# Kernel optimization log

Hardware: AMD Instinct MI355X
Metric: run time of the kernel (lower is better)

The kernel has to match this reference:

```python
import jax, jax.numpy as jnp
import numpy as np
from jax import lax


def setup_inputs() -> dict:
    key = jax.random.key(0)
    k1, k2 = jax.random.split(key)
    B, C_out, C_in, K, H, W = 16, 128, 128, 3, 64, 64
    features = jax.random.normal(k1, (B, C_in, H, W), dtype=jnp.float32)
    dynamic_kernel = jax.random.normal(k2, (B, C_out, C_in, K, K), dtype=jnp.float32)
    return {"features": features, "dynamic_kernel": dynamic_kernel}


def reference(features, dynamic_kernel):
    # Per-sample dynamic conv. unfold+bmm in torch == cross-correlation (conv2d)
    # with the per-sample kernel; we express it as a vmapped implicit-GEMM conv
    # instead of materializing the (C_in*K*K, H*W) unfold buffer.
    padding = 1

    def conv_one(x, w):  # x: (C_in, H, W), w: (C_out, C_in, K, K)
        return lax.conv_general_dilated(
            x[None],                      # (1, C_in, H, W)
            w,
            window_strides=(1, 1),
            padding=[(padding, padding), (padding, padding)],
            dimension_numbers=("NCHW", "OIHW", "NCHW"),
        )[0]                              # (C_out, H, W)

    return jax.vmap(conv_one)(features, dynamic_kernel)  # (B, C_out, H, W)
```

## Files before the change

kernel.cpp:

```cpp
#include <hip/hip_runtime.h>
#include <stdint.h>

#define BATCH 16
#define CIN   128
#define COUT  128
#define IMG_H 64
#define IMG_W 64
#define HW    4096
#define KTOT  1152
#define XH    66
#define XW    66
#define NCQ   16
#define BM    128
#define BN    64
#define BK    64
#define NSTEPS 18
#define ASTEP 8192
#define BSTEP 4096

typedef __attribute__((ext_vector_type(8))) __bf16 bf16x8;
typedef __attribute__((ext_vector_type(4))) float  f32x4;
typedef __attribute__((address_space(1))) const void* gas_p;
typedef __attribute__((address_space(3))) void*       las_p;

static __device__ __forceinline__ unsigned short f2bf(float f) {
  union { float f; uint32_t u; } c; c.f = f;
  uint32_t r = c.u + 0x7fffu + ((c.u >> 16) & 1u);
  return (unsigned short)(r >> 16);
}

static __device__ __forceinline__ void gload_lds16(const unsigned short* g, unsigned short* l) {
  __builtin_amdgcn_global_load_lds((gas_p)g, (las_p)l, 16, 0, 0);
}

__global__ void prep_fused(const float* __restrict__ x, const float* __restrict__ w,
                           unsigned short* __restrict__ wt4, unsigned short* __restrict__ xpad) {
  const int t = threadIdx.x;
  if (blockIdx.x < BATCH * IMG_H) {
    __shared__ uint32_t tile[64 * 68];
    const int b = blockIdx.x & 15;
    const int h = blockIdx.x >> 4;
    const float* xb = x + (size_t)b * CIN * HW + h * IMG_W;
    uint4* xp4 = (uint4*)xpad;

    const int lane16 = t & 15;
    const int g      = t >> 4;
#pragma unroll
    for (int it = 0; it < 4; ++it) {
      const int ci = it * 32 + g * 2;
      const float4 va = *(const float4*)(xb + (size_t)ci * HW + lane16 * 4);
      const float4 vb = *(const float4*)(xb + (size_t)(ci + 1) * HW + lane16 * 4);
      const float av[4] = {va.x, va.y, va.z, va.w};
      const float bv[4] = {vb.x, vb.y, vb.z, vb.w};
#pragma unroll
      for (int cc = 0; cc < 4; ++cc)
        tile[(lane16 * 4 + cc) * 68 + it * 16 + g] =
            (uint32_t)f2bf(av[cc]) | ((uint32_t)f2bf(bv[cc]) << 16);
    }
    __syncthreads();

    const uint32_t rbase = ((uint32_t)b * XH + h + 1) * NCQ;
#pragma unroll
    for (int it = 0; it < 4; ++it) {
      const int o   = it * 256 + t;
      const int cqg = o >> 6;
      const int wc  = o & 63;
      const uint4 v = *(const uint4*)&tile[wc * 68 + cqg * 4];
      xp4[(rbase + cqg) * XW + wc + 1] = v;
    }
    if (t < 32) {
      const int cqg = t & 15;
      const int col = (t >> 4) ? 65 : 0;
      xp4[(rbase + cqg) * XW + col] = make_uint4(0, 0, 0, 0);
    }
    if (h == 0) {
      const uint32_t r0  = (uint32_t)b * XH * NCQ * XW;
      const uint32_t r65 = ((uint32_t)b * XH + 65) * NCQ * XW;
      for (int i = t; i < NCQ * XW; i += 256) {
        xp4[r0 + i]  = make_uint4(0, 0, 0, 0);
        xp4[r65 + i] = make_uint4(0, 0, 0, 0);
      }
    }
  } else {
    const int idx  = blockIdx.x - BATCH * IMG_H;
    const int b    = idx & 15;
    const int step = idx >> 4;
    const int khkw = step >> 1;
    const int cib  = (step & 1) << 6;
    const float* wb = w + (size_t)b * COUT * KTOT;
    unsigned short* dst = wt4 + ((size_t)b * NSTEPS + step) * ASTEP;
#pragma unroll
    for (int i = 0; i < 4; ++i) {
      const int c  = i * 256 + t;
      const int cq = c >> 7;
      const int co = c & 127;
      const int ci0 = cib + cq * 8;
      const float* src = wb + (size_t)co * KTOT + (size_t)ci0 * 9 + khkw;
      uint32_t p[4];
#pragma unroll
      for (int e = 0; e < 4; ++e)
        p[e] = (uint32_t)f2bf(src[(2 * e) * 9]) | ((uint32_t)f2bf(src[(2 * e + 1) * 9]) << 16);
      *(uint4*)&dst[(size_t)c * 8] = make_uint4(p[0], p[1], p[2], p[3]);
    }
  }
}

__global__ __launch_bounds__(256, 4) void dynconv_gemm(
    const unsigned short* __restrict__ wt4,
    const unsigned short* __restrict__ xpad,
    float* __restrict__ out) {
  __shared__ alignas(16) unsigned short As[ASTEP];
  __shared__ alignas(16) unsigned short Bs[BSTEP];

  const int t    = threadIdx.x;
  const int b    = blockIdx.x & 15;
  const int oh   = blockIdx.x >> 4;

  const int lane = t & 63;
  const int wave = t >> 6;
  const int wm   = (wave & 1) << 6;
  const int wn   = (wave >> 1) << 5;
  const int l15  = lane & 15;
  const int quad = lane >> 4;

  const unsigned short* abase = wt4 + (size_t)b * NSTEPS * ASTEP + (size_t)t * 8;
  const unsigned short* xb = xpad + (size_t)b * XH * NCQ * XW * 8;
  const unsigned short* bbase[2];
#pragma unroll
  for (int i = 0; i < 2; ++i)
    bbase[i] = xb + (size_t)(((i * 4 + wave) * XW) + lane) * 8;

  unsigned short* alds[4];
  unsigned short* blds[2];
#pragma unroll
  for (int i = 0; i < 4; ++i) alds[i] = &As[(i * 256 + wave * 64) * 8];
#pragma unroll
  for (int i = 0; i < 2; ++i) blds[i] = &Bs[((i * 4 + wave) * 64) * 8];

  f32x4 acc[4][2] = {};

  for (int step = 0; step < NSTEPS; ++step) {
    const int khkw = step >> 1;
    const int kh   = (khkw * 11) >> 5;
    const int kw   = khkw - kh * 3;
    const size_t boff = ((size_t)((oh + kh) * NCQ + ((step & 1) << 3)) * XW + kw) * 8;
    const unsigned short* astep = abase + (size_t)step * ASTEP;

#pragma unroll
    for (int i = 0; i < 4; ++i) gload_lds16(astep + i * 2048, alds[i]);
#pragma unroll
    for (int i = 0; i < 2; ++i) gload_lds16(bbase[i] + boff, blds[i]);
    __syncthreads();

#pragma unroll
    for (int ks = 0; ks < 2; ++ks) {
      const int cq = ks * 4 + quad;
      bf16x8 af[4], bf[2];
#pragma unroll
      for (int i = 0; i < 4; ++i) af[i] = *(const bf16x8*)&As[(cq * 128 + wm + i * 16 + l15) * 8];
#pragma unroll
      for (int j = 0; j < 2; ++j) bf[j] = *(const bf16x8*)&Bs[(cq * 64 + wn + j * 16 + l15) * 8];
#pragma unroll
      for (int i = 0; i < 4; ++i)
#pragma unroll
        for (int j = 0; j < 2; ++j)
          acc[i][j] = __builtin_amdgcn_mfma_f32_16x16x32_bf16(af[i], bf[j], acc[i][j], 0, 0, 0);
    }
    __syncthreads();
  }

  float* obase = out + (size_t)b * COUT * HW + oh * 64;
#pragma unroll
  for (int i = 0; i < 4; ++i) {
#pragma unroll
    for (int r = 0; r < 4; ++r) {
      const int row = wm + i * 16 + quad * 4 + r;
      float* orow = obase + (size_t)row * HW;
#pragma unroll
      for (int j = 0; j < 2; ++j)
        orow[wn + j * 16 + l15] = acc[i][j][r];
    }
  }
}

__global__ void dynconv_naive(const float* __restrict__ x, const float* __restrict__ w,
                              float* __restrict__ out) {
  const int o   = blockIdx.x * 256 + threadIdx.x;
  const int pix = o & (HW - 1);
  const int co  = (o >> 12) & (COUT - 1);
  const int b   = o >> 19;
  const int oh  = pix >> 6, ow = pix & 63;
  const float* xb = x + (size_t)b * CIN * HW;
  const float* wb = w + ((size_t)b * COUT + co) * CIN * 9;
  float s = 0.f;
  for (int ci = 0; ci < CIN; ++ci) {
    const float* xc = xb + ci * HW;
    const float* wc = wb + ci * 9;
#pragma unroll
    for (int kh = 0; kh < 3; ++kh) {
      const int ih = oh + kh - 1;
      if ((unsigned)ih >= IMG_H) continue;
#pragma unroll
      for (int kw = 0; kw < 3; ++kw) {
        const int iw = ow + kw - 1;
        if ((unsigned)iw >= IMG_W) continue;
        s += xc[ih * IMG_W + iw] * wc[kh * 3 + kw];
      }
    }
  }
  out[o] = s;
}

extern "C" void kernel_launch(void* const* d_in, const int* in_sizes, int n_in,
                              void* d_out, int out_size, void* d_ws, size_t ws_size,
                              hipStream_t stream) {
  const float* x = (const float*)d_in[0];
  const float* w = (const float*)d_in[1];
  float* out = (float*)d_out;

  const size_t wt_bytes = (size_t)BATCH * NSTEPS * ASTEP * sizeof(unsigned short);
  const size_t xp_bytes = (size_t)BATCH * XH * NCQ * XW * 8 * sizeof(unsigned short);

  if (ws_size >= wt_bytes + xp_bytes) {
    unsigned short* wt4  = (unsigned short*)d_ws;
    unsigned short* xpad = (unsigned short*)((char*)d_ws + wt_bytes);
    prep_fused<<<BATCH * IMG_H + BATCH * NSTEPS, 256, 0, stream>>>(x, w, wt4, xpad);
    dynconv_gemm<<<IMG_H * BATCH, 256, 0, stream>>>(wt4, xpad, out);
  } else {
    dynconv_naive<<<(BATCH * COUT * HW) / 256, 256, 0, stream>>>(x, w, out);
  }
}
```

Measured before the change: 123.7 us.

## Stage input slab once in LDS, stream weights into registers with double buffering

Each GEMM block now covers two output rows. It loads the four padded input rows it needs (all channels) into LDS once and takes the kw shifts from that slab with clamped and zeroed edge columns, so it no longer reloads the B tile every step. Weight fragments are read directly from global memory into registers with a two-deep software pipeline, which removes the per-step LDS staging and the two barriers per step. The cost is higher register pressure (16 accumulators, 16 A fragments), occupancy dropping to 2 blocks per CU, and half as many blocks.

```diff
diff --git a/kernel.cpp b/kernel.cpp
--- a/kernel.cpp
+++ b/kernel.cpp
@@ -11,12 +11,8 @@
 #define XH    66
 #define XW    66
 #define NCQ   16
-#define BM    128
-#define BN    64
-#define BK    64
 #define NSTEPS 18
 #define ASTEP 8192
-#define BSTEP 4096
 
 typedef __attribute__((ext_vector_type(8))) __bf16 bf16x8;
 typedef __attribute__((ext_vector_type(4))) float  f32x4;
@@ -27,6 +23,11 @@
   union { float f; uint32_t u; } c; c.f = f;
   uint32_t r = c.u + 0x7fffu + ((c.u >> 16) & 1u);
   return (unsigned short)(r >> 16);
+}
+
+static __device__ __forceinline__ bf16x8 ldg8(const unsigned short* p) {
+  uint4 w = *(const uint4*)p;
+  return __builtin_bit_cast(bf16x8, w);
 }
 
 static __device__ __forceinline__ void gload_lds16(const unsigned short* g, unsigned short* l) {
@@ -105,80 +106,90 @@
   }
 }
 
-__global__ __launch_bounds__(256, 4) void dynconv_gemm(
+__global__ __launch_bounds__(256, 2) void dynconv_gemm(
     const unsigned short* __restrict__ wt4,
     const unsigned short* __restrict__ xpad,
     float* __restrict__ out) {
-  __shared__ alignas(16) unsigned short As[ASTEP];
-  __shared__ alignas(16) unsigned short Bs[BSTEP];
+  __shared__ alignas(16) unsigned short slab[4 * NCQ * 64 * 8];
 
   const int t    = threadIdx.x;
-  const int b    = blockIdx.x & 15;
-  const int oh   = blockIdx.x >> 4;
+  const int b    = blockIdx.y;
+  const int oh0  = blockIdx.x * 2;
 
   const int lane = t & 63;
   const int wave = t >> 6;
   const int wm   = (wave & 1) << 6;
-  const int wn   = (wave >> 1) << 5;
+  const int osub = wave >> 1;
   const int l15  = lane & 15;
   const int quad = lane >> 4;
 
-  const unsigned short* abase = wt4 + (size_t)b * NSTEPS * ASTEP + (size_t)t * 8;
-  const unsigned short* xb = xpad + (size_t)b * XH * NCQ * XW * 8;
-  const unsigned short* bbase[2];
-#pragma unroll
-  for (int i = 0; i < 2; ++i)
-    bbase[i] = xb + (size_t)(((i * 4 + wave) * XW) + lane) * 8;
-
-  unsigned short* alds[4];
-  unsigned short* blds[2];
-#pragma unroll
-  for (int i = 0; i < 4; ++i) alds[i] = &As[(i * 256 + wave * 64) * 8];
-#pragma unroll
-  for (int i = 0; i < 2; ++i) blds[i] = &Bs[((i * 4 + wave) * 64) * 8];
-
-  f32x4 acc[4][2] = {};
-
-  for (int step = 0; step < NSTEPS; ++step) {
-    const int khkw = step >> 1;
-    const int kh   = (khkw * 11) >> 5;
-    const int kw   = khkw - kh * 3;
-    const size_t boff = ((size_t)((oh + kh) * NCQ + ((step & 1) << 3)) * XW + kw) * 8;
-    const unsigned short* astep = abase + (size_t)step * ASTEP;
-
-#pragma unroll
-    for (int i = 0; i < 4; ++i) gload_lds16(astep + i * 2048, alds[i]);
-#pragma unroll
-    for (int i = 0; i < 2; ++i) gload_lds16(bbase[i] + boff, blds[i]);
-    __syncthreads();
-
-#pragma unroll
-    for (int ks = 0; ks < 2; ++ks) {
-      const int cq = ks * 4 + quad;
-      bf16x8 af[4], bf[2];
-#pragma unroll
-      for (int i = 0; i < 4; ++i) af[i] = *(const bf16x8*)&As[(cq * 128 + wm + i * 16 + l15) * 8];
-#pragma unroll
-      for (int j = 0; j < 2; ++j) bf[j] = *(const bf16x8*)&Bs[(cq * 64 + wn + j * 16 + l15) * 8];
-#pragma unroll
-      for (int i = 0; i < 4; ++i)
-#pragma unroll
-        for (int j = 0; j < 2; ++j)
-          acc[i][j] = __builtin_amdgcn_mfma_f32_16x16x32_bf16(af[i], bf[j], acc[i][j], 0, 0, 0);
-    }
-    __syncthreads();
-  }
-
-  float* obase = out + (size_t)b * COUT * HW + oh * 64;
+  {
+    const unsigned short* xsrc = xpad +
+        ((((size_t)b * XH + oh0) * NCQ) * XW + 1 + lane) * 8;
+#pragma unroll
+    for (int p = 0; p < 16; ++p) {
+      const int seg = p * 4 + wave;
+      gload_lds16(xsrc + (size_t)seg * XW * 8, &slab[(p * 256 + wave * 64) * 8]);
+    }
+  }
+  __syncthreads();
+
+  const unsigned short* wbase = wt4 + (size_t)b * NSTEPS * ASTEP + (size_t)(quad * 128 + wm + l15) * 8;
+
+  f32x4 acc[4][4] = {};
+  bf16x8 afA[8], afB[8];
+
+#define LOADA(S, AF)                                                          \
+  {                                                                           \
+    const unsigned short* wstep_ = wbase + (size_t)(S) * ASTEP;               \
+    _Pragma("unroll") for (int ks_ = 0; ks_ < 2; ++ks_)                       \
+      _Pragma("unroll") for (int i_ = 0; i_ < 4; ++i_)                        \
+        AF[ks_ * 4 + i_] = ldg8(wstep_ + (ks_ * 512 + i_ * 16) * 8);          \
+  }
+
+#define COMPUTE(S, AF)                                                        \
+  {                                                                           \
+    const int khkw_ = (S) >> 1;                                               \
+    const int kh_ = khkw_ / 3, kw_ = khkw_ % 3;                               \
+    _Pragma("unroll") for (int ks_ = 0; ks_ < 2; ++ks_) {                     \
+      const int cq_ = ((S) & 1) * 8 + ks_ * 4 + quad;                         \
+      const int rb_ = ((osub + kh_) * NCQ + cq_) * 64;                        \
+      bf16x8 bf[4];                                                           \
+      _Pragma("unroll") for (int j_ = 0; j_ < 4; ++j_) {                      \
+        int cm_ = j_ * 16 + l15 + kw_ - 1;                                    \
+        if (j_ == 0) cm_ = cm_ < 0 ? 0 : cm_;                                 \
+        if (j_ == 3) cm_ = cm_ > 63 ? 63 : cm_;                               \
+        bf[j_] = *(const bf16x8*)&slab[(rb_ + cm_) * 8];                      \
+      }                                                                       \
+      if (kw_ == 0 && l15 == 0)  bf[0] = (bf16x8){};                          \
+      if (kw_ == 2 && l15 == 15) bf[3] = (bf16x8){};                          \
+      _Pragma("unroll") for (int i_ = 0; i_ < 4; ++i_)                        \
+        _Pragma("unroll") for (int j_ = 0; j_ < 4; ++j_)                      \
+          acc[i_][j_] = __builtin_amdgcn_mfma_f32_16x16x32_bf16(              \
+              AF[ks_ * 4 + i_], bf[j_], acc[i_][j_], 0, 0, 0);                \
+    }                                                                         \
+  }
+
+  LOADA(0, afA);
+#pragma unroll
+  for (int s = 0; s < NSTEPS; s += 2) {
+    LOADA(s + 1, afB);
+    COMPUTE(s, afA);
+    if (s + 2 < NSTEPS) LOADA(s + 2, afA);
+    COMPUTE(s + 1, afB);
+  }
+#undef LOADA
+#undef COMPUTE
+
+  float* obase = out + (size_t)b * COUT * HW + (oh0 + osub) * 64;
 #pragma unroll
   for (int i = 0; i < 4; ++i) {
 #pragma unroll
     for (int r = 0; r < 4; ++r) {
-      const int row = wm + i * 16 + quad * 4 + r;
-      float* orow = obase + (size_t)row * HW;
-#pragma unroll
-      for (int j = 0; j < 2; ++j)
-        orow[wn + j * 16 + l15] = acc[i][j][r];
+      float* orow = obase + (size_t)(wm + i * 16 + quad * 4 + r) * HW;
+#pragma unroll
+      for (int j = 0; j < 4; ++j)
+        orow[j * 16 + l15] = acc[i][j][r];
     }
   }
 }
@@ -225,7 +236,8 @@
     unsigned short* wt4  = (unsigned short*)d_ws;
     unsigned short* xpad = (unsigned short*)((char*)d_ws + wt_bytes);
     prep_fused<<<BATCH * IMG_H + BATCH * NSTEPS, 256, 0, stream>>>(x, w, wt4, xpad);
-    dynconv_gemm<<<IMG_H * BATCH, 256, 0, stream>>>(wt4, xpad, out);
+    dim3 grid(IMG_H / 2, BATCH);
+    dynconv_gemm<<<grid, 256, 0, stream>>>(wt4, xpad, out);
   } else {
     dynconv_naive<<<(BATCH * COUT * HW) / 256, 256, 0, stream>>>(x, w, out);
   }
```

Result: slower. 131.9 us (+6.6%).
